# Optimization experiments

Measured on AMD Instinct MI355X. Metric: run time of the kernel, lower is better.

The kernel has to match this reference:

```python
import jax, jax.numpy as jnp
import numpy as np

VOCAB_SIZE = 32000
HIDDEN_DIM = 1024
NUM_BUF_ACTIONS = 128
BATCH = 64
SEQ_LEN = 512


def setup_inputs() -> dict:
    key = jax.random.key(0)
    ks = jax.random.split(key, 8)
    H = HIDDEN_DIM
    x = jax.random.randint(ks[0], (BATCH, SEQ_LEN), 0, VOCAB_SIZE, dtype=jnp.int32)
    true_actions = jax.random.randint(ks[1], (BATCH, SEQ_LEN), 0, NUM_BUF_ACTIONS, dtype=jnp.int32)
    true_states = jax.random.randint(ks[2], (BATCH, SEQ_LEN), 0, NUM_BUF_ACTIONS, dtype=jnp.int32)
    use_forcing = 0
    # Learned params: embedding table, LSTM input/recurrent kernels (gate order i,f,g,o), dense head
    embed = jax.random.normal(ks[3], (VOCAB_SIZE, H), dtype=jnp.float32) * 0.02
    Wi = jax.random.normal(ks[4], (H, 4 * H), dtype=jnp.float32) * (1.0 / np.sqrt(H))
    Wh = jax.random.normal(ks[5], (H, 4 * H), dtype=jnp.float32) * (1.0 / np.sqrt(H))
    bh = jnp.zeros((4 * H,), dtype=jnp.float32)
    Wo = jax.random.normal(ks[6], (H, NUM_BUF_ACTIONS), dtype=jnp.float32) * (1.0 / np.sqrt(H))
    bo = jnp.zeros((NUM_BUF_ACTIONS,), dtype=jnp.float32)
    return {"embed": embed, "Wi": Wi, "Wh": Wh, "bh": bh, "Wo": Wo, "bo": bo,
            "x": x, "true_actions": true_actions, "true_states": true_states,
            "use_forcing": use_forcing}


def _lstm_forward(embed, Wi, Wh, bh, Wo, bo, x):
    B, S = x.shape
    H = embed.shape[1]
    x_emb = embed[x]                                    # [B,S,H]
    # Precompute input-side gate projections for all timesteps (one big GEMM)
    gx = jnp.einsum('bsh,hg->sbg', x_emb, Wi)           # [S,B,4H]
    c0 = jnp.zeros((B, H), dtype=x_emb.dtype)
    h0 = jnp.zeros((B, H), dtype=x_emb.dtype)

    def step(carry, gx_t):
        c, h = carry
        gates = gx_t + h @ Wh + bh                      # [B,4H]
        i, f, g, o = jnp.split(gates, 4, axis=-1)
        i = jax.nn.sigmoid(i)
        f = jax.nn.sigmoid(f)
        g = jnp.tanh(g)
        o = jax.nn.sigmoid(o)
        c = f * c + i * g
        h = o * jnp.tanh(c)
        return (c, h), h

    _, hs = jax.lax.scan(step, (c0, h0), gx)            # hs: [S,B,H]
    hs = jnp.transpose(hs, (1, 0, 2))                   # [B,S,H]
    logits_buf = hs @ Wo + bo                           # [B,S,A]
    dummy = jnp.zeros((B, S, 1), dtype=logits_buf.dtype)
    return dummy, logits_buf, dummy


def reference(embed, Wi, Wh, bh, Wo, bo, x, true_actions, true_states, use_forcing):
    # true_actions/true_states/use_forcing are unused in the original forward
    return _lstm_forward(embed, Wi, Wh, bh, Wo, bo, x)
```

## Files before the change

### kernel.cpp

```cpp
#include <hip/hip_runtime.h>
#include <hip/hip_bf16.h>

typedef __attribute__((ext_vector_type(8))) short short8;
typedef __attribute__((ext_vector_type(4))) float float4v;
typedef __attribute__((ext_vector_type(4))) unsigned int uint4v;
typedef unsigned short ushort_t;
typedef unsigned int uint_t;

#define BB 64
#define SS 512
#define HH 1024
#define AA 128
#define NWG 256

#define XSW_BYTES   67108864ULL
#define WSW_BYTES   16777216ULL
#define HALL_BYTES  67239936ULL
#define XSW_OFF     0ULL
#define WSW_OFF     (XSW_OFF + XSW_BYTES)
#define HALL_OFF    (WSW_OFF + WSW_BYTES)
#define FLAGS_OFF   (HALL_OFF + HALL_BYTES)

__device__ __forceinline__ ushort_t f2bf(float f) {
    union { float f; uint_t u; } v; v.f = f;
    uint_t u = v.u;
    return (ushort_t)((u + 0x7fffu + ((u >> 16) & 1u)) >> 16);
}

__device__ __forceinline__ float fast_sigmoid(float x) {
    return __builtin_amdgcn_rcpf(1.0f + __expf(-x));
}
__device__ __forceinline__ float fast_tanh(float x) {
    return 1.0f - 2.0f * __builtin_amdgcn_rcpf(1.0f + __expf(2.0f * x));
}

__global__ void k_init(uint_t* __restrict__ flags, ushort_t* __restrict__ hall,
                       float* __restrict__ out) {
    int i = blockIdx.x * 256 + threadIdx.x;
    if (i < NWG) flags[i] = 0u;
    ((uint_t*)hall)[i] = 0u;
    out[i] = 0.0f;
    out[32768 + (size_t)BB * SS * AA + i] = 0.0f;
}

__global__ void k_prep_x(const float* __restrict__ embed, const int* __restrict__ x,
                         ushort_t* __restrict__ xsw) {
    int t = blockIdx.x * 256 + threadIdx.x;
    int lane = t & 63;
    int rg   = (t >> 6) & 3;
    int kk   = (t >> 8) & 31;
    int s    = t >> 13;
    int b  = rg * 16 + (lane & 15);
    int k0 = kk * 32 + (lane >> 4) * 8;
    int tok = x[b * SS + s];
    const float* src = embed + (size_t)tok * HH + k0;
    float4v v0 = *(const float4v*)src;
    float4v v1 = *(const float4v*)(src + 4);
    uint_t p0 = (uint_t)f2bf(v0[0]) | ((uint_t)f2bf(v0[1]) << 16);
    uint_t p1 = (uint_t)f2bf(v0[2]) | ((uint_t)f2bf(v0[3]) << 16);
    uint_t p2 = (uint_t)f2bf(v1[0]) | ((uint_t)f2bf(v1[1]) << 16);
    uint_t p3 = (uint_t)f2bf(v1[2]) | ((uint_t)f2bf(v1[3]) << 16);
    uint4v pk = {p0, p1, p2, p3};
    ((uint4v*)xsw)[t] = pk;
}

__global__ void k_prep_w(const float* __restrict__ Wi, const float* __restrict__ Wh,
                         ushort_t* __restrict__ wsw) {
    int t = blockIdx.x * 256 + threadIdx.x;
    int u = t & 1023;
    int q = (t >> 10) & 3;
    int k = t >> 12;
    float v = (k < 1024) ? Wi[(size_t)k * 4096 + q * 1024 + u]
                         : Wh[(size_t)(k - 1024) * 4096 + q * 1024 + u];
    int g = u >> 2, du = u & 3;
    int c = du * 4 + q;
    int kk = k >> 5, quad = (k >> 3) & 3, j = k & 7;
    int lane = quad * 16 + c;
    wsw[(((size_t)g * 64 + kk) * 64 + lane) * 8 + j] = f2bf(v);
}

__global__ void __launch_bounds__(256)
k_lstm(const ushort_t* __restrict__ xsw, const ushort_t* __restrict__ wsw,
       ushort_t* hall, const float* __restrict__ bh, uint_t* flags) {
    __shared__ ushort_t wlds[64 * 64 * 8];
    const int g    = blockIdx.x;
    const int tid  = threadIdx.x;
    const int lane = tid & 63;
    const int rg   = tid >> 6;

    {
        const uint4v* src = (const uint4v*)(wsw + (size_t)g * 64 * 64 * 8);
        uint4v* dst = (uint4v*)wlds;
        for (int i = tid; i < 4096; i += 256) dst[i] = src[i];
    }
    __syncthreads();

    const int c_idx = lane & 15;
    const int q  = c_idx & 3;
    const int du = c_idx >> 2;
    const int quad = lane >> 4;
    const int u = g * 4 + du;
    const float bhv = bh[q * 1024 + u];

    const int kk_h = u >> 5;
    const int quad_h = (u & 31) >> 3;
    const int j_h = u & 7;
    uint_t* hall32 = (uint_t*)hall;

    float cst0 = 0.f, cst1 = 0.f, cst2 = 0.f, cst3 = 0.f;
    const short8* xbase = (const short8*)xsw;
    const short8* hbase = (const short8*)hall;
    const short8* wl = (const short8*)wlds + lane;

    for (int s = 0; s < SS; ++s) {
        float4v ac0 = {bhv, bhv, bhv, bhv};
        float4v ac1 = {0.f, 0.f, 0.f, 0.f};
        float4v ac2 = {0.f, 0.f, 0.f, 0.f};
        float4v ac3 = {0.f, 0.f, 0.f, 0.f};

        const short8* xp = xbase + (((size_t)s * 32) * 4 + rg) * 64 + lane;
        #pragma unroll
        for (int kk = 0; kk < 32; kk += 4) {
            short8 a0 = xp[(kk + 0) * 256];
            short8 a1 = xp[(kk + 1) * 256];
            short8 a2 = xp[(kk + 2) * 256];
            short8 a3 = xp[(kk + 3) * 256];
            ac0 = __builtin_amdgcn_mfma_f32_16x16x32_bf16(a0, wl[(kk + 0) * 64], ac0, 0, 0, 0);
            ac1 = __builtin_amdgcn_mfma_f32_16x16x32_bf16(a1, wl[(kk + 1) * 64], ac1, 0, 0, 0);
            ac2 = __builtin_amdgcn_mfma_f32_16x16x32_bf16(a2, wl[(kk + 2) * 64], ac2, 0, 0, 0);
            ac3 = __builtin_amdgcn_mfma_f32_16x16x32_bf16(a3, wl[(kk + 3) * 64], ac3, 0, 0, 0);
        }

        {
            bool ok;
            do {
                uint_t f = __hip_atomic_load(&flags[tid], __ATOMIC_RELAXED,
                                             __HIP_MEMORY_SCOPE_AGENT);
                ok = (f >= (uint_t)s);
            } while (!__syncthreads_and(ok));
            asm volatile("" ::: "memory");
        }

        const short8* hp = hbase + (((size_t)s * 32) * 4 + rg) * 64 + lane;
        #pragma unroll
        for (int kk = 0; kk < 32; kk += 4) {
            short8 a0 = hp[(kk + 0) * 256];
            short8 a1 = hp[(kk + 1) * 256];
            short8 a2 = hp[(kk + 2) * 256];
            short8 a3 = hp[(kk + 3) * 256];
            ac0 = __builtin_amdgcn_mfma_f32_16x16x32_bf16(a0, wl[(32 + kk + 0) * 64], ac0, 0, 0, 0);
            ac1 = __builtin_amdgcn_mfma_f32_16x16x32_bf16(a1, wl[(32 + kk + 1) * 64], ac1, 0, 0, 0);
            ac2 = __builtin_amdgcn_mfma_f32_16x16x32_bf16(a2, wl[(32 + kk + 2) * 64], ac2, 0, 0, 0);
            ac3 = __builtin_amdgcn_mfma_f32_16x16x32_bf16(a3, wl[(32 + kk + 3) * 64], ac3, 0, 0, 0);
        }
        float4v acc = (ac0 + ac1) + (ac2 + ac3);

        float hv[4];
        #pragma unroll
        for (int r = 0; r < 4; ++r) {
            float own = acc[r];
            float a = (q == 2) ? fast_tanh(own) : fast_sigmoid(own);
            float x1 = __shfl_xor(a, 1);
            float x2 = __shfl_xor(a, 2);
            float x3 = __shfl_xor(a, 3);
            float gi, gf, gg, go;
            if      (q == 0) { gi = a;  gf = x1; gg = x2; go = x3; }
            else if (q == 1) { gi = x1; gf = a;  gg = x3; go = x2; }
            else if (q == 2) { gi = x2; gf = x3; gg = a;  go = x1; }
            else             { gi = x3; gf = x2; gg = x1; go = a;  }
            float cv = (r == 0 ? cst0 : r == 1 ? cst1 : r == 2 ? cst2 : cst3);
            cv = gf * cv + gi * gg;
            if (r == 0) cst0 = cv; else if (r == 1) cst1 = cv;
            else if (r == 2) cst2 = cv; else cst3 = cv;
            hv[r] = go * fast_tanh(cv);
        }

        float pv0 = __shfl_xor(hv[0], 4);
        float pv1 = __shfl_xor(hv[1], 4);
        float pv2 = __shfl_xor(hv[2], 4);
        float pv3 = __shfl_xor(hv[3], 4);
        if (q == 0 && (du & 1) == 0) {
            float pv[4] = {pv0, pv1, pv2, pv3};
            size_t base = (((size_t)(s + 1) * 32 + kk_h) * 4 + rg) * 64;
            #pragma unroll
            for (int r = 0; r < 4; ++r) {
                uint_t packed = (uint_t)f2bf(hv[r]) | ((uint_t)f2bf(pv[r]) << 16);
                int lane_h = quad_h * 16 + quad * 4 + r;
                size_t idx = ((base + (size_t)lane_h) * 8 + j_h) >> 1;
                __hip_atomic_store(&hall32[idx], packed, __ATOMIC_RELAXED,
                                   __HIP_MEMORY_SCOPE_AGENT);
            }
        }
        __syncthreads();
        if (tid == 0)
            __hip_atomic_store(&flags[g], (uint_t)(s + 1), __ATOMIC_RELAXED,
                               __HIP_MEMORY_SCOPE_AGENT);
    }
}

__global__ void __launch_bounds__(256)
k_head(const ushort_t* __restrict__ hall, const float* __restrict__ Wo,
       const float* __restrict__ bo, float* __restrict__ out) {
    __shared__ ushort_t wlds[32 * 2 * 64 * 8];
    const int wg = blockIdx.x;
    const int cg = wg & 3, sg = wg >> 2;
    const int tid = threadIdx.x, lane = tid & 63, rg = tid >> 6;
    const int col0 = cg * 32;

    for (int i = tid; i < 32768; i += 256) {
        int k = i >> 5;
        int col = i & 31;
        float v = Wo[(size_t)k * AA + col0 + col];
        int kk = k >> 5, quad = (k >> 3) & 3, j = k & 7;
        int nt = col >> 4, cl = col & 15;
        wlds[(((kk * 2 + nt) * 64) + quad * 16 + cl) * 8 + j] = f2bf(v);
    }
    __syncthreads();

    const int cl = lane & 15, quad = lane >> 4;
    const float bo0 = bo[col0 + cl];
    const float bo1 = bo[col0 + 16 + cl];
    const short8* wl = (const short8*)wlds + lane;

    for (int si = 0; si < 4; ++si) {
        int s = sg * 4 + si;
        float4v a0 = {bo0, bo0, bo0, bo0};
        float4v a1 = {bo1, bo1, bo1, bo1};
        const short8* hp = (const short8*)hall + (((size_t)(s + 1) * 32) * 4 + rg) * 64 + lane;
        #pragma unroll 8
        for (int kk = 0; kk < 32; ++kk) {
            short8 a = hp[kk * 256];
            a0 = __builtin_amdgcn_mfma_f32_16x16x32_bf16(a, wl[(kk * 2 + 0) * 64], a0, 0, 0, 0);
            a1 = __builtin_amdgcn_mfma_f32_16x16x32_bf16(a, wl[(kk * 2 + 1) * 64], a1, 0, 0, 0);
        }
        #pragma unroll
        for (int r = 0; r < 4; ++r) {
            int b = rg * 16 + quad * 4 + r;
            size_t o = 32768 + ((size_t)b * SS + s) * AA;
            out[o + col0 + cl]      = a0[r];
            out[o + col0 + 16 + cl] = a1[r];
        }
    }
}

extern "C" void kernel_launch(void* const* d_in, const int* in_sizes, int n_in,
                              void* d_out, int out_size, void* d_ws, size_t ws_size,
                              hipStream_t stream) {
    const float* embed = (const float*)d_in[0];
    const float* Wi    = (const float*)d_in[1];
    const float* Wh    = (const float*)d_in[2];
    const float* bh    = (const float*)d_in[3];
    const float* Wo    = (const float*)d_in[4];
    const float* bo    = (const float*)d_in[5];
    const int*   x     = (const int*)d_in[6];
    float* out = (float*)d_out;
    unsigned char* ws = (unsigned char*)d_ws;

    ushort_t* xsw  = (ushort_t*)(ws + XSW_OFF);
    ushort_t* wsw  = (ushort_t*)(ws + WSW_OFF);
    ushort_t* hall = (ushort_t*)(ws + HALL_OFF);
    uint_t*   flags = (uint_t*)(ws + FLAGS_OFF);

    k_init  <<<128,   256, 0, stream>>>(flags, hall, out);
    k_prep_x<<<16384, 256, 0, stream>>>(embed, x, xsw);
    k_prep_w<<<32768, 256, 0, stream>>>(Wi, Wh, wsw);
    k_lstm  <<<NWG,   256, 0, stream>>>(xsw, wsw, hall, bh, flags);
    k_head  <<<512,   256, 0, stream>>>(hall, Wo, bo, out);
}
```

Before: 2.804 ms.

## Replace workgroup barrier sync with per-wave flags and sentinel-polled hidden state

The recurrent kernel now signals progress per wavefront instead of per workgroup, dropping the trailing __syncthreads and having each wave poll 1024 flags spread over four loads per lane. Workgroup-level agreement now goes through small LDS atomics. The hidden-state buffer is pre-filled with a sentinel bf16 pair, so readers can re-poll individual slots until real data arrives. Produced values that happen to equal the sentinel are nudged to avoid collisions. The head kernel also polls for the sentinel, and init now writes the whole hidden-state buffer, adding a large extra memory-fill pass.

```diff
diff --git a/kernel.cpp b/kernel.cpp
--- a/kernel.cpp
+++ b/kernel.cpp
@@ -12,6 +12,8 @@
 #define HH 1024
 #define AA 128
 #define NWG 256
+
+#define SENT 0x80008000u
 
 #define XSW_BYTES   67108864ULL
 #define WSW_BYTES   16777216ULL
@@ -34,13 +36,15 @@
     return 1.0f - 2.0f * __builtin_amdgcn_rcpf(1.0f + __expf(2.0f * x));
 }
 
-__global__ void k_init(uint_t* __restrict__ flags, ushort_t* __restrict__ hall,
+__global__ void k_init(uint_t* __restrict__ flags, uint_t* __restrict__ hall32,
                        float* __restrict__ out) {
     int i = blockIdx.x * 256 + threadIdx.x;
-    if (i < NWG) flags[i] = 0u;
-    ((uint_t*)hall)[i] = 0u;
-    out[i] = 0.0f;
-    out[32768 + (size_t)BB * SS * AA + i] = 0.0f;
+    hall32[i] = (i < 32768) ? 0u : SENT;
+    if (i < 1024) flags[i] = 0u;
+    if (i < 32768) {
+        out[i] = 0.0f;
+        out[32768 + (size_t)BB * SS * AA + i] = 0.0f;
+    }
 }
 
 __global__ void k_prep_x(const float* __restrict__ embed, const int* __restrict__ x,
@@ -79,15 +83,17 @@
     wsw[(((size_t)g * 64 + kk) * 64 + lane) * 8 + j] = f2bf(v);
 }
 
-__global__ void __launch_bounds__(256)
+__global__ void __launch_bounds__(256, 1)
 k_lstm(const ushort_t* __restrict__ xsw, const ushort_t* __restrict__ wsw,
        ushort_t* hall, const float* __restrict__ bh, uint_t* flags) {
     __shared__ ushort_t wlds[64 * 64 * 8];
+    __shared__ int lds_ok[4];
     const int g    = blockIdx.x;
     const int tid  = threadIdx.x;
     const int lane = tid & 63;
     const int rg   = tid >> 6;
 
+    if (tid < 4) lds_ok[tid] = -1;
     {
         const uint4v* src = (const uint4v*)(wsw + (size_t)g * 64 * 64 * 8);
         uint4v* dst = (uint4v*)wlds;
@@ -101,6 +107,7 @@
     const int quad = lane >> 4;
     const int u = g * 4 + du;
     const float bhv = bh[q * 1024 + u];
+    const int wid = g * 4 + rg;
 
     const int kk_h = u >> 5;
     const int quad_h = (u & 31) >> 3;
@@ -109,8 +116,9 @@
 
     float cst0 = 0.f, cst1 = 0.f, cst2 = 0.f, cst3 = 0.f;
     const short8* xbase = (const short8*)xsw;
-    const short8* hbase = (const short8*)hall;
+    const uint4v* hbase4 = (const uint4v*)hall;
     const short8* wl = (const short8*)wlds + lane;
+    const uint_t* fp = flags + rg * 256 + lane;
 
     for (int s = 0; s < SS; ++s) {
         float4v ac0 = {bhv, bhv, bhv, bhv};
@@ -132,30 +140,74 @@
         }
 
         {
-            bool ok;
-            do {
-                uint_t f = __hip_atomic_load(&flags[tid], __ATOMIC_RELAXED,
-                                             __HIP_MEMORY_SCOPE_AGENT);
-                ok = (f >= (uint_t)s);
-            } while (!__syncthreads_and(ok));
-            asm volatile("" ::: "memory");
-        }
-
-        const short8* hp = hbase + (((size_t)s * 32) * 4 + rg) * 64 + lane;
-        #pragma unroll
-        for (int kk = 0; kk < 32; kk += 4) {
-            short8 a0 = hp[(kk + 0) * 256];
-            short8 a1 = hp[(kk + 1) * 256];
-            short8 a2 = hp[(kk + 2) * 256];
-            short8 a3 = hp[(kk + 3) * 256];
-            ac0 = __builtin_amdgcn_mfma_f32_16x16x32_bf16(a0, wl[(32 + kk + 0) * 64], ac0, 0, 0, 0);
-            ac1 = __builtin_amdgcn_mfma_f32_16x16x32_bf16(a1, wl[(32 + kk + 1) * 64], ac1, 0, 0, 0);
-            ac2 = __builtin_amdgcn_mfma_f32_16x16x32_bf16(a2, wl[(32 + kk + 2) * 64], ac2, 0, 0, 0);
-            ac3 = __builtin_amdgcn_mfma_f32_16x16x32_bf16(a3, wl[(32 + kk + 3) * 64], ac3, 0, 0, 0);
+            for (;;) {
+                uint_t f0 = __hip_atomic_load(fp +   0, __ATOMIC_RELAXED, __HIP_MEMORY_SCOPE_AGENT);
+                uint_t f1 = __hip_atomic_load(fp +  64, __ATOMIC_RELAXED, __HIP_MEMORY_SCOPE_AGENT);
+                uint_t f2 = __hip_atomic_load(fp + 128, __ATOMIC_RELAXED, __HIP_MEMORY_SCOPE_AGENT);
+                uint_t f3 = __hip_atomic_load(fp + 192, __ATOMIC_RELAXED, __HIP_MEMORY_SCOPE_AGENT);
+                uint_t mn = min(min(f0, f1), min(f2, f3));
+                if (__all(mn >= (uint_t)s)) break;
+            }
+            if (lane == 0)
+                __hip_atomic_store(&lds_ok[rg], s, __ATOMIC_RELAXED, __HIP_MEMORY_SCOPE_WORKGROUP);
+            for (;;) {
+                int a0 = __hip_atomic_load(&lds_ok[0], __ATOMIC_RELAXED, __HIP_MEMORY_SCOPE_WORKGROUP);
+                int a1 = __hip_atomic_load(&lds_ok[1], __ATOMIC_RELAXED, __HIP_MEMORY_SCOPE_WORKGROUP);
+                int a2 = __hip_atomic_load(&lds_ok[2], __ATOMIC_RELAXED, __HIP_MEMORY_SCOPE_WORKGROUP);
+                int a3 = __hip_atomic_load(&lds_ok[3], __ATOMIC_RELAXED, __HIP_MEMORY_SCOPE_WORKGROUP);
+                if (min(min(a0, a1), min(a2, a3)) >= s) break;
+            }
+        }
+
+        const uint4v* hp4 = hbase4 + (((size_t)s * 32) * 4 + rg) * 64 + lane;
+        uint4v h[32];
+        #pragma unroll
+        for (int m = 0; m < 32; ++m) h[m] = hp4[m * 256];
+
+        uint_t dirty = 0;
+        #pragma unroll
+        for (int m = 0; m < 32; ++m) {
+            uint_t d = (h[m][0] == SENT) | (h[m][1] == SENT) |
+                       (h[m][2] == SENT) | (h[m][3] == SENT);
+            dirty |= d << m;
+        }
+        while (__any(dirty != 0)) {
+            #pragma unroll
+            for (int m = 0; m < 32; ++m) {
+                if (dirty & (1u << m)) {
+                    const uint_t* p = (const uint_t*)(hp4 + (size_t)m * 256);
+                    h[m][0] = __hip_atomic_load(p + 0, __ATOMIC_RELAXED, __HIP_MEMORY_SCOPE_AGENT);
+                    h[m][1] = __hip_atomic_load(p + 1, __ATOMIC_RELAXED, __HIP_MEMORY_SCOPE_AGENT);
+                    h[m][2] = __hip_atomic_load(p + 2, __ATOMIC_RELAXED, __HIP_MEMORY_SCOPE_AGENT);
+                    h[m][3] = __hip_atomic_load(p + 3, __ATOMIC_RELAXED, __HIP_MEMORY_SCOPE_AGENT);
+                }
+            }
+            uint_t nd = 0;
+            #pragma unroll
+            for (int m = 0; m < 32; ++m) {
+                if (dirty & (1u << m)) {
+                    uint_t d = (h[m][0] == SENT) | (h[m][1] == SENT) |
+                               (h[m][2] == SENT) | (h[m][3] == SENT);
+                    nd |= d << m;
+                }
+            }
+            dirty = nd;
+        }
+
+        #pragma unroll
+        for (int m = 0; m < 32; m += 4) {
+            short8 a0 = __builtin_bit_cast(short8, h[m + 0]);
+            short8 a1 = __builtin_bit_cast(short8, h[m + 1]);
+            short8 a2 = __builtin_bit_cast(short8, h[m + 2]);
+            short8 a3 = __builtin_bit_cast(short8, h[m + 3]);
+            ac0 = __builtin_amdgcn_mfma_f32_16x16x32_bf16(a0, wl[(32 + m + 0) * 64], ac0, 0, 0, 0);
+            ac1 = __builtin_amdgcn_mfma_f32_16x16x32_bf16(a1, wl[(32 + m + 1) * 64], ac1, 0, 0, 0);
+            ac2 = __builtin_amdgcn_mfma_f32_16x16x32_bf16(a2, wl[(32 + m + 2) * 64], ac2, 0, 0, 0);
+            ac3 = __builtin_amdgcn_mfma_f32_16x16x32_bf16(a3, wl[(32 + m + 3) * 64], ac3, 0, 0, 0);
         }
         float4v acc = (ac0 + ac1) + (ac2 + ac3);
 
-        float hv[4];
+        size_t hsbase = (((size_t)(s + 1) * 32 + kk_h) * 4 + rg) * 64;
         #pragma unroll
         for (int r = 0; r < 4; ++r) {
             float own = acc[r];
@@ -172,28 +224,19 @@
             cv = gf * cv + gi * gg;
             if (r == 0) cst0 = cv; else if (r == 1) cst1 = cv;
             else if (r == 2) cst2 = cv; else cst3 = cv;
-            hv[r] = go * fast_tanh(cv);
-        }
-
-        float pv0 = __shfl_xor(hv[0], 4);
-        float pv1 = __shfl_xor(hv[1], 4);
-        float pv2 = __shfl_xor(hv[2], 4);
-        float pv3 = __shfl_xor(hv[3], 4);
-        if (q == 0 && (du & 1) == 0) {
-            float pv[4] = {pv0, pv1, pv2, pv3};
-            size_t base = (((size_t)(s + 1) * 32 + kk_h) * 4 + rg) * 64;
-            #pragma unroll
-            for (int r = 0; r < 4; ++r) {
-                uint_t packed = (uint_t)f2bf(hv[r]) | ((uint_t)f2bf(pv[r]) << 16);
+            float hv = go * fast_tanh(cv);
+            float pv = __shfl_xor(hv, 4);
+            if (q == 0 && (du & 1) == 0) {
+                uint_t packed = (uint_t)f2bf(hv) | ((uint_t)f2bf(pv) << 16);
+                if (packed == SENT) packed = 0x80000000u;
                 int lane_h = quad_h * 16 + quad * 4 + r;
-                size_t idx = ((base + (size_t)lane_h) * 8 + j_h) >> 1;
+                size_t idx = ((hsbase + (size_t)lane_h) * 8 + j_h) >> 1;
                 __hip_atomic_store(&hall32[idx], packed, __ATOMIC_RELAXED,
                                    __HIP_MEMORY_SCOPE_AGENT);
             }
         }
-        __syncthreads();
-        if (tid == 0)
-            __hip_atomic_store(&flags[g], (uint_t)(s + 1), __ATOMIC_RELAXED,
+        if (lane == 0)
+            __hip_atomic_store(&flags[wid], (uint_t)(s + 1), __ATOMIC_RELAXED,
                                __HIP_MEMORY_SCOPE_AGENT);
     }
 }
@@ -221,15 +264,25 @@
     const float bo0 = bo[col0 + cl];
     const float bo1 = bo[col0 + 16 + cl];
     const short8* wl = (const short8*)wlds + lane;
+    const uint4v* hbase4 = (const uint4v*)hall;
 
     for (int si = 0; si < 4; ++si) {
         int s = sg * 4 + si;
         float4v a0 = {bo0, bo0, bo0, bo0};
         float4v a1 = {bo1, bo1, bo1, bo1};
-        const short8* hp = (const short8*)hall + (((size_t)(s + 1) * 32) * 4 + rg) * 64 + lane;
+        const uint4v* hp4 = hbase4 + (((size_t)(s + 1) * 32) * 4 + rg) * 64 + lane;
         #pragma unroll 8
         for (int kk = 0; kk < 32; ++kk) {
-            short8 a = hp[kk * 256];
+            uint4v hv4 = hp4[kk * 256];
+            while (__any(((hv4[0] == SENT) | (hv4[1] == SENT) |
+                          (hv4[2] == SENT) | (hv4[3] == SENT)) != 0)) {
+                const uint_t* p = (const uint_t*)(hp4 + (size_t)kk * 256);
+                hv4[0] = __hip_atomic_load(p + 0, __ATOMIC_RELAXED, __HIP_MEMORY_SCOPE_AGENT);
+                hv4[1] = __hip_atomic_load(p + 1, __ATOMIC_RELAXED, __HIP_MEMORY_SCOPE_AGENT);
+                hv4[2] = __hip_atomic_load(p + 2, __ATOMIC_RELAXED, __HIP_MEMORY_SCOPE_AGENT);
+                hv4[3] = __hip_atomic_load(p + 3, __ATOMIC_RELAXED, __HIP_MEMORY_SCOPE_AGENT);
+            }
+            short8 a = __builtin_bit_cast(short8, hv4);
             a0 = __builtin_amdgcn_mfma_f32_16x16x32_bf16(a, wl[(kk * 2 + 0) * 64], a0, 0, 0, 0);
             a1 = __builtin_amdgcn_mfma_f32_16x16x32_bf16(a, wl[(kk * 2 + 1) * 64], a1, 0, 0, 0);
         }
@@ -261,7 +314,7 @@
     ushort_t* hall = (ushort_t*)(ws + HALL_OFF);
     uint_t*   flags = (uint_t*)(ws + FLAGS_OFF);
 
-    k_init  <<<128,   256, 0, stream>>>(flags, hall, out);
+    k_init  <<<65664, 256, 0, stream>>>(flags, (uint_t*)hall, out);
     k_prep_x<<<16384, 256, 0, stream>>>(embed, x, xsw);
     k_prep_w<<<32768, 256, 0, stream>>>(Wi, Wh, wsw);
     k_lstm  <<<NWG,   256, 0, stream>>>(xsw, wsw, hall, bh, flags);
```

Measured after the change: 6.517 ms. +132.4%, slower.

## Replace per-step workgroup barriers with wave-level LDS counter and single-wave flag polling

Applied to the files above, without the earlier changes.

Drops the per-timestep __syncthreads_and spin and the trailing __syncthreads. Each wave now bumps an LDS counter, and the last wave to arrive publishes the global step flag. Only wave 0 polls the 256 global flags (four loads per lane, with s_sleep between polls) and signals the other waves through an LDS variable. The aim is to cut barrier and global-polling overhead on the serial recurrence critical path. In exchange it depends on subtle memory-ordering guarantees: relaxed stores to hall followed by a workgroup-scope fence before an agent-scope relaxed flag store, which risks visibility races.

```diff
diff --git a/kernel.cpp b/kernel.cpp
--- a/kernel.cpp
+++ b/kernel.cpp
@@ -34,11 +34,11 @@
     return 1.0f - 2.0f * __builtin_amdgcn_rcpf(1.0f + __expf(2.0f * x));
 }
 
-__global__ void k_init(uint_t* __restrict__ flags, ushort_t* __restrict__ hall,
+__global__ void k_init(uint_t* __restrict__ flags, uint_t* __restrict__ hall32,
                        float* __restrict__ out) {
     int i = blockIdx.x * 256 + threadIdx.x;
     if (i < NWG) flags[i] = 0u;
-    ((uint_t*)hall)[i] = 0u;
+    hall32[i] = 0u;
     out[i] = 0.0f;
     out[32768 + (size_t)BB * SS * AA + i] = 0.0f;
 }
@@ -79,15 +79,18 @@
     wsw[(((size_t)g * 64 + kk) * 64 + lane) * 8 + j] = f2bf(v);
 }
 
-__global__ void __launch_bounds__(256)
+__global__ void __launch_bounds__(256, 1)
 k_lstm(const ushort_t* __restrict__ xsw, const ushort_t* __restrict__ wsw,
        ushort_t* hall, const float* __restrict__ bh, uint_t* flags) {
     __shared__ ushort_t wlds[64 * 64 * 8];
+    __shared__ int lds_ok;
+    __shared__ uint_t ctr;
     const int g    = blockIdx.x;
     const int tid  = threadIdx.x;
     const int lane = tid & 63;
     const int rg   = tid >> 6;
 
+    if (tid == 0) { lds_ok = -1; ctr = 0u; }
     {
         const uint4v* src = (const uint4v*)(wsw + (size_t)g * 64 * 64 * 8);
         uint4v* dst = (uint4v*)wlds;
@@ -111,6 +114,7 @@
     const short8* xbase = (const short8*)xsw;
     const short8* hbase = (const short8*)hall;
     const short8* wl = (const short8*)wlds + lane;
+    const uint_t* fp = flags + lane;
 
     for (int s = 0; s < SS; ++s) {
         float4v ac0 = {bhv, bhv, bhv, bhv};
@@ -131,15 +135,34 @@
             ac3 = __builtin_amdgcn_mfma_f32_16x16x32_bf16(a3, wl[(kk + 3) * 64], ac3, 0, 0, 0);
         }
 
-        {
-            bool ok;
-            do {
-                uint_t f = __hip_atomic_load(&flags[tid], __ATOMIC_RELAXED,
-                                             __HIP_MEMORY_SCOPE_AGENT);
-                ok = (f >= (uint_t)s);
-            } while (!__syncthreads_and(ok));
+        if (s > 0) {
             asm volatile("" ::: "memory");
-        }
+            __threadfence_block();
+            if (lane == 0) {
+                uint_t old = __hip_atomic_fetch_add(&ctr, 1u, __ATOMIC_ACQ_REL,
+                                                    __HIP_MEMORY_SCOPE_WORKGROUP);
+                if (old == (uint_t)(4 * s - 1))
+                    __hip_atomic_store(&flags[g], (uint_t)s, __ATOMIC_RELAXED,
+                                       __HIP_MEMORY_SCOPE_AGENT);
+            }
+        }
+
+        if (rg == 0) {
+            for (;;) {
+                uint_t f0 = __hip_atomic_load(fp +   0, __ATOMIC_RELAXED, __HIP_MEMORY_SCOPE_AGENT);
+                uint_t f1 = __hip_atomic_load(fp +  64, __ATOMIC_RELAXED, __HIP_MEMORY_SCOPE_AGENT);
+                uint_t f2 = __hip_atomic_load(fp + 128, __ATOMIC_RELAXED, __HIP_MEMORY_SCOPE_AGENT);
+                uint_t f3 = __hip_atomic_load(fp + 192, __ATOMIC_RELAXED, __HIP_MEMORY_SCOPE_AGENT);
+                uint_t mn = min(min(f0, f1), min(f2, f3));
+                if (__all(mn >= (uint_t)s)) break;
+                __builtin_amdgcn_s_sleep(1);
+            }
+            if (lane == 0)
+                __hip_atomic_store(&lds_ok, s, __ATOMIC_RELAXED, __HIP_MEMORY_SCOPE_WORKGROUP);
+        } else {
+            while (__hip_atomic_load(&lds_ok, __ATOMIC_RELAXED, __HIP_MEMORY_SCOPE_WORKGROUP) < s) {}
+        }
+        asm volatile("" ::: "memory");
 
         const short8* hp = hbase + (((size_t)s * 32) * 4 + rg) * 64 + lane;
         #pragma unroll
@@ -191,9 +214,15 @@
                                    __HIP_MEMORY_SCOPE_AGENT);
             }
         }
-        __syncthreads();
-        if (tid == 0)
-            __hip_atomic_store(&flags[g], (uint_t)(s + 1), __ATOMIC_RELAXED,
+    }
+
+    asm volatile("" ::: "memory");
+    __threadfence_block();
+    if (lane == 0) {
+        uint_t old = __hip_atomic_fetch_add(&ctr, 1u, __ATOMIC_ACQ_REL,
+                                            __HIP_MEMORY_SCOPE_WORKGROUP);
+        if (old == (uint_t)(4 * SS - 1))
+            __hip_atomic_store(&flags[g], (uint_t)SS, __ATOMIC_RELAXED,
                                __HIP_MEMORY_SCOPE_AGENT);
     }
 }
@@ -261,7 +290,7 @@
     ushort_t* hall = (ushort_t*)(ws + HALL_OFF);
     uint_t*   flags = (uint_t*)(ws + FLAGS_OFF);
 
-    k_init  <<<128,   256, 0, stream>>>(flags, hall, out);
+    k_init  <<<128,   256, 0, stream>>>(flags, (uint_t*)hall, out);
     k_prep_x<<<16384, 256, 0, stream>>>(embed, x, xsw);
     k_prep_w<<<32768, 256, 0, stream>>>(Wi, Wh, wsw);
     k_lstm  <<<NWG,   256, 0, stream>>>(xsw, wsw, hall, bh, flags);
```

Result: slower. 5.047 ms (+80.0%).

## Replace workgroup barriers with per-wave flag polling and LDS epoch counters

Applied to the files above, without the earlier changes.

Removes the __syncthreads-based barriers in the persistent LSTM recurrence. Each wave now polls its own 64 slice of the global flags, publishes a per-wave epoch in LDS, and begins consuming the h chunk it verified itself while waiting on the other waves' epochs for the remaining chunks. The per-step global flag is now raised by the last wave to increment an LDS counter instead of after a full block barrier. This is meant to let waves run out of lockstep and cut barrier latency on the serial critical path, at the cost of subtler memory-ordering reasoning with only relaxed atomics and block fences.

```diff
diff --git a/kernel.cpp b/kernel.cpp
--- a/kernel.cpp
+++ b/kernel.cpp
@@ -34,11 +34,11 @@
     return 1.0f - 2.0f * __builtin_amdgcn_rcpf(1.0f + __expf(2.0f * x));
 }
 
-__global__ void k_init(uint_t* __restrict__ flags, ushort_t* __restrict__ hall,
+__global__ void k_init(uint_t* __restrict__ flags, uint_t* __restrict__ hall32,
                        float* __restrict__ out) {
     int i = blockIdx.x * 256 + threadIdx.x;
     if (i < NWG) flags[i] = 0u;
-    ((uint_t*)hall)[i] = 0u;
+    hall32[i] = 0u;
     out[i] = 0.0f;
     out[32768 + (size_t)BB * SS * AA + i] = 0.0f;
 }
@@ -79,15 +79,19 @@
     wsw[(((size_t)g * 64 + kk) * 64 + lane) * 8 + j] = f2bf(v);
 }
 
-__global__ void __launch_bounds__(256)
+__global__ void __launch_bounds__(256, 1)
 k_lstm(const ushort_t* __restrict__ xsw, const ushort_t* __restrict__ wsw,
        ushort_t* hall, const float* __restrict__ bh, uint_t* flags) {
     __shared__ ushort_t wlds[64 * 64 * 8];
+    __shared__ int eps[4];
+    __shared__ uint_t ctr;
     const int g    = blockIdx.x;
     const int tid  = threadIdx.x;
     const int lane = tid & 63;
     const int rg   = tid >> 6;
 
+    if (tid < 4) eps[tid] = -1;
+    if (tid == 0) ctr = 0u;
     {
         const uint4v* src = (const uint4v*)(wsw + (size_t)g * 64 * 64 * 8);
         uint4v* dst = (uint4v*)wlds;
@@ -111,6 +115,7 @@
     const short8* xbase = (const short8*)xsw;
     const short8* hbase = (const short8*)hall;
     const short8* wl = (const short8*)wlds + lane;
+    const uint_t* fp = flags + rg * 64 + lane;
 
     for (int s = 0; s < SS; ++s) {
         float4v ac0 = {bhv, bhv, bhv, bhv};
@@ -132,26 +137,39 @@
         }
 
         {
-            bool ok;
+            uint_t f;
             do {
-                uint_t f = __hip_atomic_load(&flags[tid], __ATOMIC_RELAXED,
-                                             __HIP_MEMORY_SCOPE_AGENT);
-                ok = (f >= (uint_t)s);
-            } while (!__syncthreads_and(ok));
-            asm volatile("" ::: "memory");
+                f = __hip_atomic_load(fp, __ATOMIC_RELAXED, __HIP_MEMORY_SCOPE_AGENT);
+            } while (!__all(f >= (uint_t)s));
+            if (lane == 0)
+                __hip_atomic_store(&eps[rg], s, __ATOMIC_RELAXED, __HIP_MEMORY_SCOPE_WORKGROUP);
         }
 
         const short8* hp = hbase + (((size_t)s * 32) * 4 + rg) * 64 + lane;
         #pragma unroll
-        for (int kk = 0; kk < 32; kk += 4) {
-            short8 a0 = hp[(kk + 0) * 256];
-            short8 a1 = hp[(kk + 1) * 256];
-            short8 a2 = hp[(kk + 2) * 256];
-            short8 a3 = hp[(kk + 3) * 256];
-            ac0 = __builtin_amdgcn_mfma_f32_16x16x32_bf16(a0, wl[(32 + kk + 0) * 64], ac0, 0, 0, 0);
-            ac1 = __builtin_amdgcn_mfma_f32_16x16x32_bf16(a1, wl[(32 + kk + 1) * 64], ac1, 0, 0, 0);
-            ac2 = __builtin_amdgcn_mfma_f32_16x16x32_bf16(a2, wl[(32 + kk + 2) * 64], ac2, 0, 0, 0);
-            ac3 = __builtin_amdgcn_mfma_f32_16x16x32_bf16(a3, wl[(32 + kk + 3) * 64], ac3, 0, 0, 0);
+        for (int i = 0; i < 4; ++i) {
+            int qq = (rg + i) & 3;
+            if (i > 0) {
+                while (__hip_atomic_load(&eps[qq], __ATOMIC_RELAXED,
+                                         __HIP_MEMORY_SCOPE_WORKGROUP) < s) {}
+            }
+            const int kb = qq * 8;
+            short8 a0 = hp[(kb + 0) * 256];
+            short8 a1 = hp[(kb + 1) * 256];
+            short8 a2 = hp[(kb + 2) * 256];
+            short8 a3 = hp[(kb + 3) * 256];
+            short8 a4 = hp[(kb + 4) * 256];
+            short8 a5 = hp[(kb + 5) * 256];
+            short8 a6 = hp[(kb + 6) * 256];
+            short8 a7 = hp[(kb + 7) * 256];
+            ac0 = __builtin_amdgcn_mfma_f32_16x16x32_bf16(a0, wl[(32 + kb + 0) * 64], ac0, 0, 0, 0);
+            ac1 = __builtin_amdgcn_mfma_f32_16x16x32_bf16(a1, wl[(32 + kb + 1) * 64], ac1, 0, 0, 0);
+            ac2 = __builtin_amdgcn_mfma_f32_16x16x32_bf16(a2, wl[(32 + kb + 2) * 64], ac2, 0, 0, 0);
+            ac3 = __builtin_amdgcn_mfma_f32_16x16x32_bf16(a3, wl[(32 + kb + 3) * 64], ac3, 0, 0, 0);
+            ac0 = __builtin_amdgcn_mfma_f32_16x16x32_bf16(a4, wl[(32 + kb + 4) * 64], ac0, 0, 0, 0);
+            ac1 = __builtin_amdgcn_mfma_f32_16x16x32_bf16(a5, wl[(32 + kb + 5) * 64], ac1, 0, 0, 0);
+            ac2 = __builtin_amdgcn_mfma_f32_16x16x32_bf16(a6, wl[(32 + kb + 6) * 64], ac2, 0, 0, 0);
+            ac3 = __builtin_amdgcn_mfma_f32_16x16x32_bf16(a7, wl[(32 + kb + 7) * 64], ac3, 0, 0, 0);
         }
         float4v acc = (ac0 + ac1) + (ac2 + ac3);
 
@@ -191,10 +209,16 @@
                                    __HIP_MEMORY_SCOPE_AGENT);
             }
         }
-        __syncthreads();
-        if (tid == 0)
-            __hip_atomic_store(&flags[g], (uint_t)(s + 1), __ATOMIC_RELAXED,
-                               __HIP_MEMORY_SCOPE_AGENT);
+
+        asm volatile("" ::: "memory");
+        __threadfence_block();
+        if (lane == 0) {
+            uint_t old = __hip_atomic_fetch_add(&ctr, 1u, __ATOMIC_ACQ_REL,
+                                                __HIP_MEMORY_SCOPE_WORKGROUP);
+            if (old == (uint_t)(4 * s + 3))
+                __hip_atomic_store(&flags[g], (uint_t)(s + 1), __ATOMIC_RELAXED,
+                                   __HIP_MEMORY_SCOPE_AGENT);
+        }
     }
 }
 
@@ -261,7 +285,7 @@
     ushort_t* hall = (ushort_t*)(ws + HALL_OFF);
     uint_t*   flags = (uint_t*)(ws + FLAGS_OFF);
 
-    k_init  <<<128,   256, 0, stream>>>(flags, hall, out);
+    k_init  <<<128,   256, 0, stream>>>(flags, (uint_t*)hall, out);
     k_prep_x<<<16384, 256, 0, stream>>>(embed, x, xsw);
     k_prep_w<<<32768, 256, 0, stream>>>(Wi, Wh, wsw);
     k_lstm  <<<NWG,   256, 0, stream>>>(xsw, wsw, hall, bh, flags);
```

Measured after the change: 4.775 ms. +70.3%, slower.
